# Kernel optimization log

Hardware: AMD Instinct MI355X
Metric: run time of the kernel (lower is better)

The kernel has to match this reference:

```python
import jax, jax.numpy as jnp
import numpy as np

NUM_HEADS = 16
PHI = 1.6180339887  # golden ratio, module-level constant in source repo
STRIDE = 4
LOCAL = 8  # +/- 8 local window in 'strided' pattern


def setup_inputs() -> dict:
    key = jax.random.key(0)
    ks = jax.random.split(key, 6)
    B, S, H = 2, 2048, 1024
    scale = H ** -0.5
    x = jax.random.normal(ks[0], (B, S, H), jnp.float32)
    # Linear(bias=False) weights, stored as [in, out] (equivalent to torch W.T)
    q_w = jax.random.normal(ks[1], (H, H), jnp.float32) * scale
    k_w = jax.random.normal(ks[2], (H, H), jnp.float32) * scale
    v_w = jax.random.normal(ks[3], (H, H), jnp.float32) * scale
    o_w = jax.random.normal(ks[4], (H, H), jnp.float32) * scale
    o_b = jax.random.normal(ks[5], (H,), jnp.float32) * 0.01
    unity_scale = jnp.asarray(PHI, jnp.float32)
    return {"x": x, "q_w": q_w, "k_w": k_w, "v_w": v_w,
            "o_w": o_w, "o_b": o_b, "unity_scale": unity_scale}


def _strided_allowed(S):
    # allowed[i, j] = True if j is attended from i:
    # every STRIDE-th column, OR within +/-LOCAL of the diagonal
    i = jnp.arange(S)[:, None]
    j = jnp.arange(S)[None, :]
    return ((j % STRIDE) == 0) | (jnp.abs(i - j) <= LOCAL)


def reference(x, q_w, k_w, v_w, o_w, o_b, unity_scale):
    B, S, H = x.shape
    NH = NUM_HEADS
    D = H // NH
    # QKV projections -> [B, NH, S, D]
    q = (x @ q_w).reshape(B, S, NH, D).transpose(0, 2, 1, 3)
    k = (x @ k_w).reshape(B, S, NH, D).transpose(0, 2, 1, 3)
    v = (x @ v_w).reshape(B, S, NH, D).transpose(0, 2, 1, 3)
    q = q * jax.nn.sigmoid(unity_scale)
    # sparse ('strided') attention: dense scores + mask, as in source
    scores = jnp.einsum('bhqd,bhkd->bhqk', q, k) / jnp.sqrt(jnp.asarray(D, x.dtype))
    allowed = _strided_allowed(S)  # [S, S] bool
    scores = jnp.where(allowed, scores, -jnp.inf)
    attn = jax.nn.softmax(scores, axis=-1)
    out = jnp.einsum('bhqk,bhkd->bhqd', attn, v)  # [B, NH, S, D]
    out = out.transpose(0, 2, 1, 3).reshape(B, S, H)
    return out @ o_w + o_b
```

## Files before the change

### kernel.cpp

```cpp
#include <hip/hip_runtime.h>
#include <math.h>

#define S_LEN   2048
#define HDIM    1024
#define NHEADS  16
#define DHEAD   64
#define BATCH   2
#define MROWS   (BATCH * S_LEN)
#define STRIDE  4
#define LOCAL   8
#define NSTRIDED (S_LEN / STRIDE)

typedef __attribute__((ext_vector_type(8))) _Float16 f16x8;
typedef __attribute__((ext_vector_type(4))) float f32x4;

__device__ __forceinline__ unsigned short f16b(float x) {
    _Float16 h = (_Float16)x;
    unsigned short u;
    __builtin_memcpy(&u, &h, 2);
    return u;
}
__device__ __forceinline__ unsigned pack2_f16(float a, float b) {
    return (unsigned)f16b(a) | ((unsigned)f16b(b) << 16);
}

__device__ __forceinline__ void gll16(const void* g, void* l) {
    __builtin_amdgcn_global_load_lds(
        (const __attribute__((address_space(1))) void*)g,
        (__attribute__((address_space(3))) void*)l, 16, 0, 0);
}

#define WAIT_BARRIER(N)                                             \
    do {                                                            \
        asm volatile("s_waitcnt vmcnt(" #N ")" ::: "memory");       \
        __builtin_amdgcn_s_barrier();                               \
        __builtin_amdgcn_sched_barrier(0);                          \
    } while (0)
#define READ_DONE_BARRIER()                                         \
    do {                                                            \
        __builtin_amdgcn_s_barrier();                               \
        __builtin_amdgcn_sched_barrier(0);                          \
    } while (0)

__global__ __launch_bounds__(256)
void xcvt(const float* __restrict__ src, unsigned short* __restrict__ dst, int n4)
{
    const int i = blockIdx.x * 256 + threadIdx.x;
    if (i >= n4) return;
    const float4 v = reinterpret_cast<const float4*>(src)[i];
    reinterpret_cast<ushort4*>(dst)[i] =
        make_ushort4(f16b(v.x), f16b(v.y), f16b(v.z), f16b(v.w));
}

__global__ __launch_bounds__(256)
void wcvt(const float* __restrict__ W0, const float* __restrict__ W1,
          const float* __restrict__ W2, const float* __restrict__ W3,
          unsigned short* __restrict__ dst)
{
    __shared__ unsigned short tile[32][33];
    const int z = blockIdx.z;
    const float* __restrict__ W = (z == 0) ? W0 : (z == 1) ? W1 : (z == 2) ? W2 : W3;
    unsigned short* __restrict__ out = dst + (size_t)z * HDIM * HDIM;
    const int t  = threadIdx.x;
    const int kb = blockIdx.x * 32;
    const int nb = blockIdx.y * 32;
    {
        const int row = t >> 3;
        const int c4  = (t & 7) * 4;
        const float4 v = *reinterpret_cast<const float4*>(
            &W[(size_t)(kb + row) * HDIM + nb + c4]);
        tile[row][c4 + 0] = f16b(v.x);
        tile[row][c4 + 1] = f16b(v.y);
        tile[row][c4 + 2] = f16b(v.z);
        tile[row][c4 + 3] = f16b(v.w);
    }
    __syncthreads();
    {
        const int n  = t >> 3;
        const int k4 = (t & 7) * 4;
        *reinterpret_cast<ushort4*>(&out[(size_t)(nb + n) * HDIM + kb + k4]) =
            make_ushort4(tile[k4][n], tile[k4+1][n], tile[k4+2][n], tile[k4+3][n]);
    }
}

__global__ __launch_bounds__(256)
void gemm_qkv(const unsigned short* __restrict__ A,
              const unsigned short* __restrict__ Wbase,
              const float* __restrict__ sig_ptr,
              unsigned short* __restrict__ Qf, unsigned short* __restrict__ Kf,
              unsigned short* __restrict__ Kp, unsigned short* __restrict__ Vt,
              unsigned short* __restrict__ Vpt)
{
    __shared__ unsigned short As[128 * 64];
    __shared__ unsigned short Bs[128 * 64];

    const int z = blockIdx.z;
    const unsigned short* __restrict__ WT = Wbase + (size_t)z * HDIM * HDIM;

    const int tid  = threadIdx.x;
    const int lane = tid & 63;
    const int w    = tid >> 6;
    const int wr   = w >> 1;
    const int wc   = w & 1;
    const int row_base = blockIdx.y * 128;
    const int col_base = blockIdx.x * 128;

    f32x4 acc[4][4] = {};

    auto stage = [&](int k0) {
#pragma unroll
        for (int r = 0; r < 4; ++r) {
            const int c    = tid + r * 256;
            const int row  = c >> 3;
            const int c7   = c & 7;
            const int goff = ((c7 * 16) ^ ((row & 7) << 4)) >> 1;
            gll16(A  + (size_t)(row_base + row) * HDIM + k0 + goff, &As[c * 8]);
            gll16(WT + (size_t)(col_base + row) * HDIM + k0 + goff, &Bs[c * 8]);
        }
    };

    auto compute = [&]() {
#pragma unroll
        for (int kk = 0; kk < 2; ++kk) {
            const int sofs = (kk * 64 + ((lane >> 4) << 4)) ^ ((lane & 7) << 4);
            f16x8 af[4], bfr[4];
#pragma unroll
            for (int mi = 0; mi < 4; ++mi) {
                const int row = wr * 64 + mi * 16 + (lane & 15);
                af[mi] = *reinterpret_cast<const f16x8*>(
                    reinterpret_cast<const char*>(&As[row * 64]) + sofs);
            }
#pragma unroll
            for (int ni = 0; ni < 4; ++ni) {
                const int row = wc * 64 + ni * 16 + (lane & 15);
                bfr[ni] = *reinterpret_cast<const f16x8*>(
                    reinterpret_cast<const char*>(&Bs[row * 64]) + sofs);
            }
#pragma unroll
            for (int mi = 0; mi < 4; ++mi)
#pragma unroll
                for (int ni = 0; ni < 4; ++ni)
                    acc[mi][ni] = __builtin_amdgcn_mfma_f32_16x16x32_f16(
                        af[mi], bfr[ni], acc[mi][ni], 0, 0, 0);
        }
    };

#pragma unroll 1
    for (int kt = 0; kt < 16; ++kt) {
        stage(kt * 64);
        __syncthreads();
        compute();
        __syncthreads();
    }

    float scale = 1.0f;
    if (z == 0) {
        const float u = *sig_ptr;
        scale = (1.0f / (1.0f + __expf(-u))) * 0.125f;
    }
#pragma unroll
    for (int mi = 0; mi < 4; ++mi) {
#pragma unroll
        for (int ni = 0; ni < 4; ++ni) {
            const int gr0 = row_base + wr * 64 + mi * 16 + ((lane >> 4) << 2);
            const int gc  = col_base + wc * 64 + ni * 16 + (lane & 15);
            const int h = gc >> 6, d = gc & 63;
            const int bb = gr0 >> 11;
            const int s0 = gr0 & (S_LEN - 1);
            const size_t bh = (size_t)(bb * NHEADS + h);
            if (z == 0) {
#pragma unroll
                for (int r = 0; r < 4; ++r)
                    Qf[(bh * S_LEN + s0 + r) * DHEAD + d] =
                        f16b(acc[mi][ni][r] * scale);
            } else if (z == 1) {
#pragma unroll
                for (int r = 0; r < 4; ++r)
                    Kf[(bh * S_LEN + s0 + r) * DHEAD + d] = f16b(acc[mi][ni][r]);
                Kp[(bh * NSTRIDED + (s0 >> 2)) * DHEAD + d] = f16b(acc[mi][ni][0]);
            } else {
                ushort4 pv = make_ushort4(f16b(acc[mi][ni][0]), f16b(acc[mi][ni][1]),
                                          f16b(acc[mi][ni][2]), f16b(acc[mi][ni][3]));
                *reinterpret_cast<ushort4*>(&Vt[(bh * DHEAD + d) * S_LEN + s0]) = pv;
                Vpt[(bh * DHEAD + d) * NSTRIDED + (s0 >> 2)] = pv.x;
            }
        }
    }
}

__global__ __launch_bounds__(256)
void gemm_out(const unsigned short* __restrict__ A,
              const unsigned short* __restrict__ WT,
              float* __restrict__ C, const float* __restrict__ bias)
{
    __shared__ unsigned short As[128 * 64];
    __shared__ unsigned short Bs[64 * 64];

    const int tid  = threadIdx.x;
    const int lane = tid & 63;
    const int w    = tid >> 6;
    const int wr   = w >> 1;
    const int wc   = w & 1;
    const int row_base = blockIdx.y * 128;
    const int col_base = blockIdx.x * 64;

    f32x4 acc[4][2] = {};

    auto stage = [&](int k0) {
#pragma unroll
        for (int r = 0; r < 4; ++r) {
            const int c    = tid + r * 256;
            const int row  = c >> 3;
            const int c7   = c & 7;
            const int goff = ((c7 * 16) ^ ((row & 7) << 4)) >> 1;
            gll16(A + (size_t)(row_base + row) * HDIM + k0 + goff, &As[c * 8]);
        }
#pragma unroll
        for (int r = 0; r < 2; ++r) {
            const int c    = tid + r * 256;
            const int row  = c >> 3;
            const int c7   = c & 7;
            const int goff = ((c7 * 16) ^ ((row & 7) << 4)) >> 1;
            gll16(WT + (size_t)(col_base + row) * HDIM + k0 + goff, &Bs[c * 8]);
        }
    };

    auto compute = [&]() {
#pragma unroll
        for (int kk = 0; kk < 2; ++kk) {
            const int sofs = (kk * 64 + ((lane >> 4) << 4)) ^ ((lane & 7) << 4);
            f16x8 af[4], bfr[2];
#pragma unroll
            for (int mi = 0; mi < 4; ++mi) {
                const int row = wr * 64 + mi * 16 + (lane & 15);
                af[mi] = *reinterpret_cast<const f16x8*>(
                    reinterpret_cast<const char*>(&As[row * 64]) + sofs);
            }
#pragma unroll
            for (int ni = 0; ni < 2; ++ni) {
                const int row = wc * 32 + ni * 16 + (lane & 15);
                bfr[ni] = *reinterpret_cast<const f16x8*>(
                    reinterpret_cast<const char*>(&Bs[row * 64]) + sofs);
            }
#pragma unroll
            for (int mi = 0; mi < 4; ++mi)
#pragma unroll
                for (int ni = 0; ni < 2; ++ni)
                    acc[mi][ni] = __builtin_amdgcn_mfma_f32_16x16x32_f16(
                        af[mi], bfr[ni], acc[mi][ni], 0, 0, 0);
        }
    };

#pragma unroll 1
    for (int kt = 0; kt < 16; ++kt) {
        stage(kt * 64);
        __syncthreads();
        compute();
        __syncthreads();
    }

#pragma unroll
    for (int mi = 0; mi < 4; ++mi) {
#pragma unroll
        for (int ni = 0; ni < 2; ++ni) {
            const int gr0 = row_base + wr * 64 + mi * 16 + ((lane >> 4) << 2);
            const int gc  = col_base + wc * 32 + ni * 16 + (lane & 15);
            const float bv = bias[gc];
#pragma unroll
            for (int r = 0; r < 4; ++r)
                C[(size_t)(gr0 + r) * HDIM + gc] = acc[mi][ni][r] + bv;
        }
    }
}

__global__ __launch_bounds__(256)
void attn_mfma(const unsigned short* __restrict__ Qf, const unsigned short* __restrict__ Kf,
               const unsigned short* __restrict__ Kp, const unsigned short* __restrict__ Vt,
               const unsigned short* __restrict__ Vpt,
               unsigned short* __restrict__ Of)
{
    __shared__ unsigned short Ks[2][32 * 64];
    __shared__ unsigned short Vs[2][64 * 32];
    __shared__ unsigned short P[4][2][16][40];

    const int tid = threadIdx.x;
    const int L = tid & 63, w = tid >> 6;
    const int c = L & 15, g = L >> 4;
    const int bx = blockIdx.x;
    const int bh = bx & 31;
    const int qb = bx >> 5;
    const int h  = bh & 15;
    const int b  = bh >> 4;
    const int wr0 = qb * 128 + w * 32;
    const size_t bhs = (size_t)(b * NHEADS + h);

    const unsigned short* __restrict__ Qb  = Qf  + bhs * S_LEN * DHEAD;
    const unsigned short* __restrict__ Kfb = Kf  + bhs * S_LEN * DHEAD;
    const unsigned short* __restrict__ Kpb = Kp  + bhs * NSTRIDED * DHEAD;
    const unsigned short* __restrict__ Vtb = Vt  + bhs * DHEAD * S_LEN;
    const unsigned short* __restrict__ Vpb = Vpt + bhs * DHEAD * NSTRIDED;

    f16x8 qf[2][2];
#pragma unroll
    for (int qi = 0; qi < 2; ++qi) {
        const int row = wr0 + 16 * qi + c;
        qf[qi][0] = *reinterpret_cast<const f16x8*>(&Qb[row * DHEAD + 8 * g]);
        qf[qi][1] = *reinterpret_cast<const f16x8*>(&Qb[row * DHEAD + 32 + 8 * g]);
    }

    f32x4 acc[2][4] = {};
    float m[2]  = {-1e30f, -1e30f};
    float ls[2] = {0.0f, 0.0f};

    auto stage = [&](int bsel, int t) {
        const int jj0 = t * 32;
        {
            const int row  = tid >> 3;
            const int colB = (tid & 7) * 16;
            const int src  = (colB ^ ((row & 7) << 4)) >> 1;
            gll16(Kpb + (jj0 + row) * DHEAD + src, &Ks[bsel][tid * 8]);
        }
        {
            const int d    = tid >> 2;
            const int colB = (tid & 3) * 16;
            const int src  = (colB ^ ((d & 3) << 4)) >> 1;
            gll16(Vpb + d * NSTRIDED + jj0 + src, &Vs[bsel][tid * 8]);
        }
    };

    auto softmax_pv = [&](int qi, f32x4 sc0, f32x4 sc1, const f16x8 vfr[4]) {
        float pmax = fmaxf(fmaxf(fmaxf(sc0[0], sc0[1]), fmaxf(sc0[2], sc0[3])),
                           fmaxf(fmaxf(sc1[0], sc1[1]), fmaxf(sc1[2], sc1[3])));
        pmax = fmaxf(pmax, __shfl_xor(pmax, 16));
        pmax = fmaxf(pmax, __shfl_xor(pmax, 32));
        if (__any(pmax > m[qi] + 8.0f)) {
            const float mn = fmaxf(m[qi], pmax);
            const float f  = __expf(m[qi] - mn);
            ls[qi] *= f;
#pragma unroll
            for (int dt = 0; dt < 4; ++dt)
#pragma unroll
                for (int r = 0; r < 4; ++r) acc[qi][dt][r] *= f;
            m[qi] = mn;
        }
        float p[8];
#pragma unroll
        for (int r = 0; r < 4; ++r) p[r]     = __expf(sc0[r] - m[qi]);
#pragma unroll
        for (int r = 0; r < 4; ++r) p[4 + r] = __expf(sc1[r] - m[qi]);
        ls[qi] += ((p[0] + p[1]) + (p[2] + p[3])) + ((p[4] + p[5]) + (p[6] + p[7]));

        char* const Pb = (char*)&P[w][qi][c][0];
        *reinterpret_cast<uint2*>(Pb + 8 * g) =
            make_uint2(pack2_f16(p[0], p[1]), pack2_f16(p[2], p[3]));
        *reinterpret_cast<uint2*>(Pb + 32 + 8 * g) =
            make_uint2(pack2_f16(p[4], p[5]), pack2_f16(p[6], p[7]));
        const f16x8 pf = *reinterpret_cast<const f16x8*>(Pb + 16 * g);

#pragma unroll
        for (int dt = 0; dt < 4; ++dt)
            acc[qi][dt] = __builtin_amdgcn_mfma_f32_16x16x32_f16(
                vfr[dt], pf, acc[qi][dt], 0, 0, 0);
    };

    auto chunk_from_lds = [&](int buf) {
        f16x8 kfr[2][2], vfr[4];
        const char* KsB = (const char*)&Ks[buf][0];
        const char* VsB = (const char*)&Vs[buf][0];
#pragma unroll
        for (int half = 0; half < 2; ++half)
#pragma unroll
            for (int sl = 0; sl < 2; ++sl) {
                const int addr = (half * 16 + c) * 128 +
                                 ((sl * 64 + g * 16) ^ ((c & 7) << 4));
                kfr[half][sl] = *reinterpret_cast<const f16x8*>(KsB + addr);
            }
#pragma unroll
        for (int dt = 0; dt < 4; ++dt) {
            const int d    = dt * 16 + c;
            const int addr = d * 64 + ((g * 16) ^ ((d & 3) << 4));
            vfr[dt] = *reinterpret_cast<const f16x8*>(VsB + addr);
        }
#pragma unroll
        for (int qi = 0; qi < 2; ++qi) {
            f32x4 sc0 = {}, sc1 = {};
            sc0 = __builtin_amdgcn_mfma_f32_16x16x32_f16(kfr[0][0], qf[qi][0], sc0, 0, 0, 0);
            sc0 = __builtin_amdgcn_mfma_f32_16x16x32_f16(kfr[0][1], qf[qi][1], sc0, 0, 0, 0);
            sc1 = __builtin_amdgcn_mfma_f32_16x16x32_f16(kfr[1][0], qf[qi][0], sc1, 0, 0, 0);
            sc1 = __builtin_amdgcn_mfma_f32_16x16x32_f16(kfr[1][1], qf[qi][1], sc1, 0, 0, 0);
            softmax_pv(qi, sc0, sc1, vfr);
        }
    };

    stage(0, 0);
    int buf = 0;
#pragma unroll 1
    for (int t = 0; t < 15; ++t) {
        stage(buf ^ 1, t + 1);
        WAIT_BARRIER(2);
        chunk_from_lds(buf);
        READ_DONE_BARRIER();
        buf ^= 1;
    }
    asm volatile("s_waitcnt vmcnt(0)" ::: "memory");
    __builtin_amdgcn_s_barrier();
    __builtin_amdgcn_sched_barrier(0);
    chunk_from_lds(buf);

#pragma unroll
    for (int qi = 0; qi < 2; ++qi) {
        const int j0 = wr0 + 16 * qi - LOCAL;
        f16x8 kfr[2][2], vfr[4];
#pragma unroll
        for (int half = 0; half < 2; ++half) {
            int j = j0 + half * 16 + c;
            j = min(max(j, 0), S_LEN - 1);
#pragma unroll
            for (int sl = 0; sl < 2; ++sl)
                kfr[half][sl] = *reinterpret_cast<const f16x8*>(
                    &Kfb[j * DHEAD + sl * 32 + 8 * g]);
        }
        int js = j0 + 8 * g;
        js = min(max(js, 0), S_LEN - 8);
#pragma unroll
        for (int dt = 0; dt < 4; ++dt)
            vfr[dt] = *reinterpret_cast<const f16x8*>(
                &Vtb[(dt * 16 + c) * S_LEN + js]);

        f32x4 sc0 = {}, sc1 = {};
        sc0 = __builtin_amdgcn_mfma_f32_16x16x32_f16(kfr[0][0], qf[qi][0], sc0, 0, 0, 0);
        sc0 = __builtin_amdgcn_mfma_f32_16x16x32_f16(kfr[0][1], qf[qi][1], sc0, 0, 0, 0);
        sc1 = __builtin_amdgcn_mfma_f32_16x16x32_f16(kfr[1][0], qf[qi][0], sc1, 0, 0, 0);
        sc1 = __builtin_amdgcn_mfma_f32_16x16x32_f16(kfr[1][1], qf[qi][1], sc1, 0, 0, 0);

        const int i = wr0 + 16 * qi + c;
#pragma unroll
        for (int r = 0; r < 4; ++r) {
            const int j = j0 + 4 * g + r;
            const bool ok = (j >= 0) && (j < S_LEN) && ((j & 3) != 0) &&
                            (j >= i - LOCAL) && (j <= i + LOCAL);
            if (!ok) sc0[r] = -1e30f;
        }
#pragma unroll
        for (int r = 0; r < 4; ++r) {
            const int j = j0 + 16 + 4 * g + r;
            const bool ok = (j >= 0) && (j < S_LEN) && ((j & 3) != 0) &&
                            (j >= i - LOCAL) && (j <= i + LOCAL);
            if (!ok) sc1[r] = -1e30f;
        }
        softmax_pv(qi, sc0, sc1, vfr);
    }

#pragma unroll
    for (int qi = 0; qi < 2; ++qi) {
        float lt = ls[qi];
        lt += __shfl_xor(lt, 16);
        lt += __shfl_xor(lt, 32);
        const float inv = 1.0f / lt;
        const int s = wr0 + 16 * qi + c;
        const size_t ob = ((size_t)(b * S_LEN + s)) * HDIM + h * DHEAD;
#pragma unroll
        for (int dt = 0; dt < 4; ++dt) {
            ushort4 hv = make_ushort4(
                f16b(acc[qi][dt][0] * inv), f16b(acc[qi][dt][1] * inv),
                f16b(acc[qi][dt][2] * inv), f16b(acc[qi][dt][3] * inv));
            *reinterpret_cast<ushort4*>(&Of[ob + dt * 16 + 4 * g]) = hv;
        }
    }
}

extern "C" void kernel_launch(void* const* d_in, const int* in_sizes, int n_in,
                              void* d_out, int out_size, void* d_ws, size_t ws_size,
                              hipStream_t stream)
{
    const float* x      = (const float*)d_in[0];
    const float* q_w    = (const float*)d_in[1];
    const float* k_w    = (const float*)d_in[2];
    const float* v_w    = (const float*)d_in[3];
    const float* o_w    = (const float*)d_in[4];
    const float* o_b    = (const float*)d_in[5];
    const float* uscale = (const float*)d_in[6];
    float* out = (float*)d_out;

    const size_t MB = (size_t)1 << 20;
    char* ws = (char*)d_ws;
    unsigned short* Xf   = (unsigned short*)(ws);
    unsigned short* Wall = (unsigned short*)(ws + 8 * MB);
    unsigned short* Qf   = (unsigned short*)(ws + 16 * MB);
    unsigned short* Kf   = (unsigned short*)(ws + 24 * MB);
    unsigned short* Kp   = (unsigned short*)(ws + 32 * MB);
    unsigned short* Vt   = (unsigned short*)(ws + 34 * MB);
    unsigned short* Vpt  = (unsigned short*)(ws + 42 * MB);
    unsigned short* Of   = (unsigned short*)(ws + 44 * MB);

    xcvt<<<dim3(MROWS * HDIM / 4 / 256), dim3(256), 0, stream>>>(
        x, Xf, MROWS * HDIM / 4);
    wcvt<<<dim3(HDIM / 32, HDIM / 32, 4), dim3(256), 0, stream>>>(
        q_w, k_w, v_w, o_w, Wall);

    const dim3 gg(HDIM / 128, MROWS / 128, 3);
    gemm_qkv<<<gg, dim3(256), 0, stream>>>(Xf, Wall, uscale,
                                           Qf, Kf, Kp, Vt, Vpt);

    attn_mfma<<<dim3(16 * 32), dim3(256), 0, stream>>>(
        Qf, Kf, Kp, Vt, Vpt, Of);

    const dim3 go(HDIM / 64, MROWS / 128);
    gemm_out<<<go, dim3(256), 0, stream>>>(Of, Wall + 3 * (size_t)HDIM * HDIM,
                                           out, o_b);
}
```

Baseline: 109.7 us.

## Restructure QKV GEMM into 256x256 double-buffered pipelined tiles with 512 threads

The QKV projection GEMM moves from 128x128 tiles with 4 waves and single-buffered LDS to 256x256 tiles with 8 waves, double-buffered LDS and a software pipeline. Global-to-LDS loads for the next K step are interleaved in quarters between MFMA groups, and s_setprio is raised around the MFMA bursts. The aim is to hide global load latency behind compute and raise data reuse per tile. In exchange, LDS use grows to 128KB, more registers are needed, and the grid shrinks to 192 blocks, which may underfill the 256 CUs.

```diff
diff --git a/kernel.cpp b/kernel.cpp
--- a/kernel.cpp
+++ b/kernel.cpp
@@ -30,17 +30,20 @@
         (__attribute__((address_space(3))) void*)l, 16, 0, 0);
 }
 
-#define WAIT_BARRIER(N)                                             \
-    do {                                                            \
-        asm volatile("s_waitcnt vmcnt(" #N ")" ::: "memory");       \
-        __builtin_amdgcn_s_barrier();                               \
-        __builtin_amdgcn_sched_barrier(0);                          \
-    } while (0)
-#define READ_DONE_BARRIER()                                         \
+#define VMCNT(n)  asm volatile("s_waitcnt vmcnt(" #n ")" ::: "memory")
+#define BAR()                                                       \
     do {                                                            \
         __builtin_amdgcn_s_barrier();                               \
         __builtin_amdgcn_sched_barrier(0);                          \
     } while (0)
+#define LGKM0()                                                     \
+    do {                                                            \
+        asm volatile("s_waitcnt lgkmcnt(0)" ::: "memory");          \
+        __builtin_amdgcn_sched_barrier(0);                          \
+    } while (0)
+#define WAIT_BARRIER(N)                                             \
+    do { VMCNT(N); BAR(); } while (0)
+#define READ_DONE_BARRIER() BAR()
 
 __global__ __launch_bounds__(256)
 void xcvt(const float* __restrict__ src, unsigned short* __restrict__ dst, int n4)
@@ -83,7 +86,7 @@
     }
 }
 
-__global__ __launch_bounds__(256)
+__global__ __launch_bounds__(512)
 void gemm_qkv(const unsigned short* __restrict__ A,
               const unsigned short* __restrict__ Wbase,
               const float* __restrict__ sig_ptr,
@@ -91,8 +94,8 @@
               unsigned short* __restrict__ Kp, unsigned short* __restrict__ Vt,
               unsigned short* __restrict__ Vpt)
 {
-    __shared__ unsigned short As[128 * 64];
-    __shared__ unsigned short Bs[128 * 64];
+    __shared__ unsigned short As[2][256 * 64];
+    __shared__ unsigned short Bs[2][256 * 64];
 
     const int z = blockIdx.z;
     const unsigned short* __restrict__ WT = Wbase + (size_t)z * HDIM * HDIM;
@@ -100,57 +103,125 @@
     const int tid  = threadIdx.x;
     const int lane = tid & 63;
     const int w    = tid >> 6;
-    const int wr   = w >> 1;
-    const int wc   = w & 1;
-    const int row_base = blockIdx.y * 128;
-    const int col_base = blockIdx.x * 128;
-
-    f32x4 acc[4][4] = {};
-
-    auto stage = [&](int k0) {
-#pragma unroll
-        for (int r = 0; r < 4; ++r) {
-            const int c    = tid + r * 256;
-            const int row  = c >> 3;
-            const int c7   = c & 7;
-            const int goff = ((c7 * 16) ^ ((row & 7) << 4)) >> 1;
-            gll16(A  + (size_t)(row_base + row) * HDIM + k0 + goff, &As[c * 8]);
-            gll16(WT + (size_t)(col_base + row) * HDIM + k0 + goff, &Bs[c * 8]);
-        }
-    };
-
-    auto compute = [&]() {
-#pragma unroll
-        for (int kk = 0; kk < 2; ++kk) {
-            const int sofs = (kk * 64 + ((lane >> 4) << 4)) ^ ((lane & 7) << 4);
-            f16x8 af[4], bfr[4];
-#pragma unroll
-            for (int mi = 0; mi < 4; ++mi) {
-                const int row = wr * 64 + mi * 16 + (lane & 15);
-                af[mi] = *reinterpret_cast<const f16x8*>(
-                    reinterpret_cast<const char*>(&As[row * 64]) + sofs);
-            }
-#pragma unroll
-            for (int ni = 0; ni < 4; ++ni) {
-                const int row = wc * 64 + ni * 16 + (lane & 15);
-                bfr[ni] = *reinterpret_cast<const f16x8*>(
-                    reinterpret_cast<const char*>(&Bs[row * 64]) + sofs);
-            }
-#pragma unroll
-            for (int mi = 0; mi < 4; ++mi)
-#pragma unroll
-                for (int ni = 0; ni < 4; ++ni)
-                    acc[mi][ni] = __builtin_amdgcn_mfma_f32_16x16x32_f16(
-                        af[mi], bfr[ni], acc[mi][ni], 0, 0, 0);
-        }
-    };
+    const int wr   = w >> 2;
+    const int wc   = w & 3;
+    const int row_base = blockIdx.y * 256;
+    const int col_base = blockIdx.x * 256;
+
+    f32x4 acc[8][4] = {};
+    f16x8 bf[4];
+    f16x8 af[4];
+
+    auto stageA = [&](int b, int k0, int r) {
+        const int c    = tid + r * 512;
+        const int row  = c >> 3;
+        const int c7   = c & 7;
+        const int goff = ((c7 * 16) ^ ((row & 7) << 4)) >> 1;
+        gll16(A + (size_t)(row_base + row) * HDIM + k0 + goff, &As[b][c * 8]);
+    };
+    auto stageB = [&](int b, int k0, int r) {
+        const int c    = tid + r * 512;
+        const int row  = c >> 3;
+        const int c7   = c & 7;
+        const int goff = ((c7 * 16) ^ ((row & 7) << 4)) >> 1;
+        gll16(WT + (size_t)(col_base + row) * HDIM + k0 + goff, &Bs[b][c * 8]);
+    };
+
+    auto ldA = [&](int b, int mi, int kk) -> f16x8 {
+        const int row  = wr * 128 + mi * 16 + (lane & 15);
+        const int sofs = (kk * 64 + ((lane >> 4) << 4)) ^ ((lane & 7) << 4);
+        return *reinterpret_cast<const f16x8*>(
+            reinterpret_cast<const char*>(&As[b][row * 64]) + sofs);
+    };
+    auto ldB = [&](int b, int ni, int kk) -> f16x8 {
+        const int row  = wc * 64 + ni * 16 + (lane & 15);
+        const int sofs = (kk * 64 + ((lane >> 4) << 4)) ^ ((lane & 7) << 4);
+        return *reinterpret_cast<const f16x8*>(
+            reinterpret_cast<const char*>(&Bs[b][row * 64]) + sofs);
+    };
+
+    auto mfma4x4 = [&](int mibase) {
+        __builtin_amdgcn_s_setprio(1);
+#pragma unroll
+        for (int mi = 0; mi < 4; ++mi)
+#pragma unroll
+            for (int ni = 0; ni < 4; ++ni)
+                acc[mibase + mi][ni] = __builtin_amdgcn_mfma_f32_16x16x32_f16(
+                    af[mi], bf[ni], acc[mibase + mi][ni], 0, 0, 0);
+        __builtin_amdgcn_s_setprio(0);
+    };
+
+    stageB(0, 0, 0); stageB(0, 0, 1); stageB(0, 0, 2); stageB(0, 0, 3);
+    stageA(0, 0, 0); stageA(0, 0, 2); stageA(0, 0, 1); stageA(0, 0, 3);
 
 #pragma unroll 1
-    for (int kt = 0; kt < 16; ++kt) {
-        stage(kt * 64);
-        __syncthreads();
-        compute();
-        __syncthreads();
+    for (int kt = 0; kt < 15; ++kt) {
+        const int b   = kt & 1;
+        const int nb  = b ^ 1;
+        const int nk0 = (kt + 1) * 64;
+
+        WAIT_BARRIER(2);
+#pragma unroll
+        for (int mi = 0; mi < 4; ++mi) af[mi] = ldA(b, mi, 0);
+#pragma unroll
+        for (int ni = 0; ni < 4; ++ni) bf[ni] = ldB(b, ni, 0);
+        stageB(nb, nk0, 0); stageB(nb, nk0, 1);
+        LGKM0();
+        mfma4x4(0);
+
+        WAIT_BARRIER(2);
+#pragma unroll
+        for (int mi = 0; mi < 4; ++mi) af[mi] = ldA(b, 4 + mi, 0);
+        stageB(nb, nk0, 2); stageB(nb, nk0, 3);
+        LGKM0();
+        mfma4x4(4);
+
+        BAR();
+#pragma unroll
+        for (int mi = 0; mi < 4; ++mi) af[mi] = ldA(b, mi, 1);
+#pragma unroll
+        for (int ni = 0; ni < 4; ++ni) bf[ni] = ldB(b, ni, 1);
+        stageA(nb, nk0, 0); stageA(nb, nk0, 2);
+        LGKM0();
+        mfma4x4(0);
+
+        BAR();
+#pragma unroll
+        for (int mi = 0; mi < 4; ++mi) af[mi] = ldA(b, 4 + mi, 1);
+        stageA(nb, nk0, 1); stageA(nb, nk0, 3);
+        LGKM0();
+        mfma4x4(4);
+    }
+
+    {
+        const int b = 1;
+        WAIT_BARRIER(2);
+#pragma unroll
+        for (int mi = 0; mi < 4; ++mi) af[mi] = ldA(b, mi, 0);
+#pragma unroll
+        for (int ni = 0; ni < 4; ++ni) bf[ni] = ldB(b, ni, 0);
+        LGKM0();
+        mfma4x4(0);
+
+        WAIT_BARRIER(0);
+#pragma unroll
+        for (int mi = 0; mi < 4; ++mi) af[mi] = ldA(b, 4 + mi, 0);
+        LGKM0();
+        mfma4x4(4);
+
+        BAR();
+#pragma unroll
+        for (int mi = 0; mi < 4; ++mi) af[mi] = ldA(b, mi, 1);
+#pragma unroll
+        for (int ni = 0; ni < 4; ++ni) bf[ni] = ldB(b, ni, 1);
+        LGKM0();
+        mfma4x4(0);
+
+        BAR();
+#pragma unroll
+        for (int mi = 0; mi < 4; ++mi) af[mi] = ldA(b, 4 + mi, 1);
+        LGKM0();
+        mfma4x4(4);
     }
 
     float scale = 1.0f;
@@ -159,10 +230,10 @@
         scale = (1.0f / (1.0f + __expf(-u))) * 0.125f;
     }
 #pragma unroll
-    for (int mi = 0; mi < 4; ++mi) {
+    for (int mi = 0; mi < 8; ++mi) {
 #pragma unroll
         for (int ni = 0; ni < 4; ++ni) {
-            const int gr0 = row_base + wr * 64 + mi * 16 + ((lane >> 4) << 2);
+            const int gr0 = row_base + wr * 128 + mi * 16 + ((lane >> 4) << 2);
             const int gc  = col_base + wc * 64 + ni * 16 + (lane & 15);
             const int h = gc >> 6, d = gc & 63;
             const int bb = gr0 >> 11;
@@ -402,9 +473,8 @@
         READ_DONE_BARRIER();
         buf ^= 1;
     }
-    asm volatile("s_waitcnt vmcnt(0)" ::: "memory");
-    __builtin_amdgcn_s_barrier();
-    __builtin_amdgcn_sched_barrier(0);
+    VMCNT(0);
+    BAR();
     chunk_from_lds(buf);
 
 #pragma unroll
@@ -498,8 +568,8 @@
     wcvt<<<dim3(HDIM / 32, HDIM / 32, 4), dim3(256), 0, stream>>>(
         q_w, k_w, v_w, o_w, Wall);
 
-    const dim3 gg(HDIM / 128, MROWS / 128, 3);
-    gemm_qkv<<<gg, dim3(256), 0, stream>>>(Xf, Wall, uscale,
+    const dim3 gg(HDIM / 256, MROWS / 256, 3);
+    gemm_qkv<<<gg, dim3(512), 0, stream>>>(Xf, Wall, uscale,
                                            Qf, Kf, Kp, Vt, Vpt);
 
     attn_mfma<<<dim3(16 * 32), dim3(256), 0, stream>>>(
```

After: 101.1 us. -7.8%, faster.
